# Kernel tuning notes

Hardware: AMD Instinct MI355X
Metric: run time of the kernel (lower is better)

## Reference

```python
import jax, jax.numpy as jnp
import numpy as np

B, D, K, DM = 4096, 64, 64, 512  # batch, latent_dim, num_charts, d_model
BALL_EPS = 1e-5


def _l2n(x):
    return x / (jnp.linalg.norm(x) + 1e-12)


def _spectral_scale(W, iters=5):
    # torch.nn.utils.spectral_norm semantics: power iteration with no-grad u,v,
    # gradient flows through W in sigma = u^T W v.
    Wd = jax.lax.stop_gradient(W)
    u = _l2n(jnp.ones((W.shape[0],), W.dtype))
    v = _l2n(Wd.T @ u)
    for _ in range(iters):
        v = _l2n(Wd.T @ u)
        u = _l2n(Wd @ v)
    sigma = u @ (W @ v)
    return W / sigma


def spectral_linear(x, W, b):
    return x @ _spectral_scale(W).T + b


def _project_to_ball(x):
    n = jnp.linalg.norm(x, axis=-1, keepdims=True)
    scale = jnp.minimum(1.0, (1.0 - BALL_EPS) / jnp.maximum(n, 1e-12))
    return x * scale


def _poincare_dist2(x, y):
    # x: [B, D] query positions, y: [B, K, D] chart centers -> squared geodesic dist [B, K]
    diff2 = jnp.sum((x[:, None, :] - y) ** 2, axis=-1)
    den = (1.0 - jnp.sum(x * x, axis=-1, keepdims=True)) * (1.0 - jnp.sum(y * y, axis=-1))
    arg = 1.0 + 2.0 * diff2 / jnp.maximum(den, 1e-12)
    d = jnp.arccosh(jnp.maximum(arg, 1.0 + 1e-7))
    return d * d


def covariant_attention(z_q, z_kv, x_q, x_k, x_v, Wq, bq, Wk, bk, Wv, bv, Wo, bo, geo_scale):
    # Single-head geodesic-biased attention (GeodesicConfig n_heads=1).
    q = x_q @ Wq.T + bq                               # [B, DM]
    k = jnp.einsum('bkd,ed->bke', x_k, Wk) + bk       # [B, K, DM]
    v = jnp.einsum('bkd,ed->bke', x_v, Wv) + bv       # [B, K, DM]
    scores = jnp.einsum('bd,bkd->bk', q, k) / jnp.sqrt(jnp.asarray(DM, q.dtype))
    scores = scores - geo_scale * _poincare_dist2(z_q, z_kv)
    attn = jax.nn.softmax(scores, axis=-1)            # [B, K]
    feat = jnp.einsum('bk,bkd->bd', attn, v)
    out = feat @ Wo.T + bo                            # [B, DM]
    return out, attn


def setup_inputs() -> dict:
    keys = jax.random.split(jax.random.key(0), 20)
    z = 0.05 * jax.random.normal(keys[0], (B, D), jnp.float32)      # inside unit ball
    rw = jax.nn.softmax(jax.random.normal(keys[1], (B, K), jnp.float32), axis=-1)
    chart_emb = 0.02 * jax.random.normal(keys[2], (K, DM), jnp.float32)
    cc = jax.random.normal(keys[3], (K, D), jnp.float32)
    chart_centers = 0.3 * (cc / jnp.linalg.norm(cc, axis=-1, keepdims=True))
    s = 0.02
    return {
        'z': z, 'rw': rw,
        'chart_emb': chart_emb, 'chart_centers': chart_centers,
        'zW': s * jax.random.normal(keys[4], (DM, D), jnp.float32),
        'zb': jnp.zeros((DM,), jnp.float32),
        'Wq': s * jax.random.normal(keys[5], (DM, DM), jnp.float32),
        'bq': jnp.zeros((DM,), jnp.float32),
        'Wk': s * jax.random.normal(keys[6], (DM, DM), jnp.float32),
        'bk': jnp.zeros((DM,), jnp.float32),
        'Wv': s * jax.random.normal(keys[7], (DM, DM), jnp.float32),
        'bv': jnp.zeros((DM,), jnp.float32),
        'Wo': s * jax.random.normal(keys[8], (DM, DM), jnp.float32),
        'bo': jnp.zeros((DM,), jnp.float32),
        'geo_scale': jnp.ones((), jnp.float32),
        'vW': s * jax.random.normal(keys[9], (1, DM), jnp.float32),
        'vb': jnp.zeros((1,), jnp.float32),
    }


def reference(z, rw, chart_emb, chart_centers, zW, zb, Wq, bq, Wk, bk, Wv, bv, Wo, bo, geo_scale, vW, vb):
    # ChartTokenizer: broadcast-multiply router weights with chart embeddings
    tokens_x = rw[:, :, None] * chart_emb[None]            # [B, K, DM]
    tokens_z = jnp.broadcast_to(_project_to_ball(chart_centers)[None], (z.shape[0], K, D))
    # z embedding (SpectralLinear)
    x_q = spectral_linear(z, zW, zb)                       # [B, DM]
    # critic covariant attention
    v_feat, _ = covariant_attention(z, tokens_z, x_q, tokens_x, tokens_x,
                                    Wq, bq, Wk, bk, Wv, bv, Wo, bo, geo_scale)
    # task value head (SpectralLinear -> scalar)
    return spectral_linear(v_feat, vW, vb)                 # [B, 1]
```

## Files before the change

### kernel.cpp

```cpp
#include <hip/hip_runtime.h>
#include <math.h>

#define WS_INV    0
#define WS_INVSV  1
#define WS_BOVW   2
#define WS_BVWO   3
#define WS_N2V    4
#define WS_COLSUM 64
#define WS_A      128
#define WS_WO0    4224
#define WS_QZB    4736
#define WS_CK0    5248
#define WS_CVW    5312
#define WS_NY2    5376
#define WS_YT     5440
#define WS_T1     16384
#define WS_V1     49152
#define WS_P1     81920
#define WS_GP     114688

#define PRE_LDSB  (36928 * 4)
#define MID_LDSB  (16384 * 4)

__device__ __forceinline__ float wave_sum(float x) {
#pragma unroll
    for (int o = 32; o; o >>= 1) x += __shfl_xor(x, o);
    return x;
}

__device__ __forceinline__ float block_sum512(float v, float* red) {
    float s = wave_sum(v);
    const int wid = threadIdx.x >> 6;
    __syncthreads();
    if ((threadIdx.x & 63) == 0) red[wid] = s;
    __syncthreads();
    float t2 = 0.0f;
#pragma unroll
    for (int i = 0; i < 8; ++i) t2 += red[i];
    return t2;
}

__global__ __launch_bounds__(512) void k_pre(
    const float* __restrict__ zW, const float* __restrict__ zb,
    const float* __restrict__ Wq, const float* __restrict__ bq,
    const float* __restrict__ Wk, const float* __restrict__ Wv,
    const float* __restrict__ Wo, const float* __restrict__ ce,
    const float* __restrict__ cc, const float* __restrict__ vW,
    const float* __restrict__ bo, float* __restrict__ ws)
{
    extern __shared__ float sm[];
    const int blk = blockIdx.x, t = threadIdx.x;
    const int lane = t & 63, w = t >> 6;

    if (blk < 128) {
        const int f0 = blk * 4;
        float* ces = sm;
        float* wkv = sm + 32832;
#pragma unroll 4
        for (int i = 0; i < 64; ++i) {
            const int idx = i * 512 + t;
            ces[(idx >> 9) * 513 + (idx & 511)] = ce[idx];
        }
        {
            const float4* Wk4 = (const float4*)Wk;
            const float4* Wv4 = (const float4*)Wv;
            float4* wkv4 = (float4*)wkv;
#pragma unroll
            for (int i = 0; i < 2; ++i) {
                const int idx = i * 512 + t;
                const int a = idx >> 7, c4 = idx & 127;
                wkv4[idx] = (a < 4) ? Wk4[(f0 + a) * 128 + c4]
                                    : Wv4[(f0 + a - 4) * 128 + c4];
            }
        }
        __syncthreads();
        float acc[8];
#pragma unroll
        for (int a = 0; a < 8; ++a) acc[a] = 0.0f;
        const int c0 = w * 64;
#pragma unroll 2
        for (int q4 = 0; q4 < 16; ++q4) {
            const int c = c0 + q4 * 4;
            const float cv0 = ces[lane * 513 + c + 0];
            const float cv1 = ces[lane * 513 + c + 1];
            const float cv2 = ces[lane * 513 + c + 2];
            const float cv3 = ces[lane * 513 + c + 3];
#pragma unroll
            for (int a = 0; a < 8; ++a) {
                const float4 wv4 = *(const float4*)&wkv[a * 512 + c];
                acc[a] = fmaf(wv4.x, cv0, acc[a]);
                acc[a] = fmaf(wv4.y, cv1, acc[a]);
                acc[a] = fmaf(wv4.z, cv2, acc[a]);
                acc[a] = fmaf(wv4.w, cv3, acc[a]);
            }
        }
        __syncthreads();
        float* part = sm;
#pragma unroll
        for (int a = 0; a < 8; ++a) part[(a * 8 + w) * 65 + lane] = acc[a];
        __syncthreads();
        {
            float s = 0.0f;
#pragma unroll
            for (int ww = 0; ww < 8; ++ww) s += part[(w * 8 + ww) * 65 + lane];
            if (w < 4) ws[WS_T1 + (f0 + w) * 64 + lane] = s;
            else       ws[WS_V1 + (f0 + w - 4) * 64 + lane] = s;
        }

    } else if (blk < 192) {
        const int f0 = (blk - 128) * 8;
        float* zl = sm;
        float* wq = sm + 32768;
        {
            const float4* zW4 = (const float4*)zW;
            float4* zl4 = (float4*)zl;
#pragma unroll 4
            for (int i = 0; i < 16; ++i) zl4[i * 512 + t] = zW4[i * 512 + t];
            const float4* Wq4 = (const float4*)Wq;
            float4* wq4 = (float4*)wq;
#pragma unroll
            for (int i = 0; i < 2; ++i)
                wq4[i * 512 + t] = Wq4[f0 * 128 + i * 512 + t];
        }
        __syncthreads();
        float acc[8];
#pragma unroll
        for (int a = 0; a < 8; ++a) acc[a] = 0.0f;
        const int e0 = w * 64;
#pragma unroll 2
        for (int q4 = 0; q4 < 16; ++q4) {
            const int e = e0 + q4 * 4;
            const float z0 = zl[(e + 0) * 64 + lane];
            const float z1 = zl[(e + 1) * 64 + lane];
            const float z2 = zl[(e + 2) * 64 + lane];
            const float z3 = zl[(e + 3) * 64 + lane];
#pragma unroll
            for (int fi = 0; fi < 8; ++fi) {
                const float4 q4v = *(const float4*)&wq[fi * 512 + e];
                acc[fi] = fmaf(q4v.x, z0, acc[fi]);
                acc[fi] = fmaf(q4v.y, z1, acc[fi]);
                acc[fi] = fmaf(q4v.z, z2, acc[fi]);
                acc[fi] = fmaf(q4v.w, z3, acc[fi]);
            }
        }
        __syncthreads();
        float* part = sm;
#pragma unroll
        for (int a = 0; a < 8; ++a) part[(a * 8 + w) * 65 + lane] = acc[a];
        __syncthreads();
        {
            float s = 0.0f;
#pragma unroll
            for (int ww = 0; ww < 8; ++ww) s += part[(w * 8 + ww) * 65 + lane];
            ws[WS_P1 + (f0 + w) * 64 + lane] = s;
        }

    } else if (blk < 200) {
        const int r0 = (blk - 192) * 8;
        float* zl = sm;
        {
            const float4* zW4 = (const float4*)zW;
            float4* zl4 = (float4*)zl;
#pragma unroll 4
            for (int i = 0; i < 16; ++i) zl4[i * 512 + t] = zW4[i * 512 + t];
        }
        __syncthreads();
        float acc[8];
#pragma unroll
        for (int a = 0; a < 8; ++a) acc[a] = 0.0f;
        float cs = 0.0f;
        const int e0 = w * 64;
#pragma unroll 2
        for (int q4 = 0; q4 < 16; ++q4) {
            const int e = e0 + q4 * 4;
#pragma unroll
            for (int j = 0; j < 4; ++j) {
                const float zv = zl[(e + j) * 64 + lane];
                cs += zv;
                const float4 b0 = *(const float4*)&zl[(e + j) * 64 + r0];
                const float4 b1 = *(const float4*)&zl[(e + j) * 64 + r0 + 4];
                acc[0] = fmaf(b0.x, zv, acc[0]);
                acc[1] = fmaf(b0.y, zv, acc[1]);
                acc[2] = fmaf(b0.z, zv, acc[2]);
                acc[3] = fmaf(b0.w, zv, acc[3]);
                acc[4] = fmaf(b1.x, zv, acc[4]);
                acc[5] = fmaf(b1.y, zv, acc[5]);
                acc[6] = fmaf(b1.z, zv, acc[6]);
                acc[7] = fmaf(b1.w, zv, acc[7]);
            }
        }
        __syncthreads();
        float* part = sm;
        float* part2 = sm + 4160;
#pragma unroll
        for (int a = 0; a < 8; ++a) part[(a * 8 + w) * 65 + lane] = acc[a];
        if (blk == 192) part2[w * 65 + lane] = cs;
        __syncthreads();
        {
            float s = 0.0f;
#pragma unroll
            for (int ww = 0; ww < 8; ++ww) s += part[(w * 8 + ww) * 65 + lane];
            ws[WS_A + (r0 + w) * 64 + lane] = s;
        }
        if (blk == 192 && t < 64) {
            float s = 0.0f;
#pragma unroll
            for (int ww = 0; ww < 8; ++ww) s += part2[ww * 65 + t];
            ws[WS_COLSUM + t] = s;
        }

    } else if (blk < 208) {
        const int f0 = (blk - 200) * 64;
        float zbr[8];
#pragma unroll
        for (int i = 0; i < 8; ++i) zbr[i] = zb[i * 64 + lane];
#pragma unroll
        for (int ff = 0; ff < 8; ++ff) {
            const int f = f0 + w * 8 + ff;
            float s = 0.0f;
#pragma unroll
            for (int i = 0; i < 8; ++i)
                s = fmaf(Wq[f * 512 + i * 64 + lane], zbr[i], s);
            s = wave_sum(s);
            if (lane == 0) ws[WS_QZB + f] = s + bq[f];
        }

    } else if (blk < 216) {
        const int e0 = (blk - 208) * 64;
        float s = 0.0f;
#pragma unroll 4
        for (int gi = 0; gi < 64; ++gi) {
            const int g = w * 64 + gi;
            s = fmaf(Wo[g * 512 + e0 + lane], vW[g], s);
        }
        float* part = sm;
        part[w * 65 + lane] = s;
        __syncthreads();
        if (t < 64) {
            float o = 0.0f;
#pragma unroll
            for (int ww = 0; ww < 8; ++ww) o += part[ww * 65 + t];
            ws[WS_WO0 + e0 + t] = o;
        }

    } else {
        float* red = sm;
        const float vwt = vW[t];
        const float n2v = block_sum512(vwt * vwt, red);
        if (t == 0) ws[WS_N2V] = n2v;
        const float bv_ = block_sum512(bo[t] * vwt, red);
        if (t == 0) ws[WS_BOVW] = bv_;
        if (t < 64) {
            float n2 = 0.0f;
            for (int dd = 0; dd < 64; ++dd) {
                const float c = cc[t * 64 + dd];
                n2 = fmaf(c, c, n2);
            }
            const float n = sqrtf(n2);
            const float scale = fminf(1.0f, (1.0f - 1e-5f) / fmaxf(n, 1e-12f));
            float s2 = 0.0f;
            for (int dd = 0; dd < 64; ++dd) {
                const float yv = cc[t * 64 + dd] * scale;
                ws[WS_YT + dd * 64 + t] = yv;
                s2 = fmaf(yv, yv, s2);
            }
            ws[WS_NY2 + t] = s2;
        }
    }
}

__global__ __launch_bounds__(512) void k_mid(
    const float* __restrict__ bv, float* __restrict__ ws)
{
    extern __shared__ float sm[];
    const int blk = blockIdx.x, t = threadIdx.x;
    const int lane = t & 63, w = t >> 6;

    if (blk == 0) {
        float* As = sm;
#pragma unroll
        for (int i = 0; i < 8; ++i) {
            const int idx = i * 512 + t;
            As[(idx >> 6) * 65 + (idx & 63)] = ws[WS_A + idx];
        }
        __syncthreads();
        if (w == 0) {
            const int d = lane;
            const float u0val = 1.0f / (sqrtf(512.0f) + 1e-12f);
            const float x = ws[WS_COLSUM + d] * u0val;
            const float nx = sqrtf(wave_sum(x * x));
            float v = x / (nx + 1e-12f);
            float mv;
            for (int it = 0; it < 4; ++it) {
                mv = 0.0f;
                for (int j = 0; j < 64; ++j)
                    mv = fmaf(As[j * 65 + d], __shfl(v, j), mv);
                const float s1 = wave_sum(mv * v);
                const float s2 = wave_sum(mv * mv);
                const float n = sqrtf(s1);
                const float inv1 = 1.0f / (n + 1e-12f);
                const float ny = sqrtf(s2) * inv1;
                v = mv * inv1 / (ny + 1e-12f);
            }
            mv = 0.0f;
            for (int j = 0; j < 64; ++j)
                mv = fmaf(As[j * 65 + d], __shfl(v, j), mv);
            const float n5sq = wave_sum(mv * v);
            const float n5 = sqrtf(n5sq);
            const float sig = n5sq / (n5 + 1e-12f);
            if (lane == 0) ws[WS_INV] = 1.0f / sig;
        } else if (w == 1) {
            float s = 0.0f;
#pragma unroll
            for (int i = 0; i < 8; ++i)
                s = fmaf(bv[i * 64 + lane], ws[WS_WO0 + i * 64 + lane], s);
            s = wave_sum(s);
            if (lane == 0) ws[WS_BVWO] = s;
        } else if (w == 2 && lane == 0) {
            const float n2 = ws[WS_N2V];
            const float rn = sqrtf(n2);
            float u = 1.0f / (1.0f + 1e-12f), s = 0.0f;
            for (int it = 0; it < 5; ++it) {
                const float nv = fabsf(u) * rn;
                const float vs = u / (nv + 1e-12f);
                s = n2 * vs;
                u = s / (fabsf(s) + 1e-12f);
            }
            ws[WS_INVSV] = 1.0f / (u * s);
        }

    } else if (blk < 3) {
        const int mat = (blk == 1) ? WS_V1 : WS_T1;
        const int vec = (blk == 1) ? WS_WO0 : WS_QZB;
        const int dst = (blk == 1) ? WS_CVW : WS_CK0;
        float s = 0.0f;
#pragma unroll 4
        for (int i = 0; i < 64; ++i) {
            const int e = w * 64 + i;
            s = fmaf(ws[mat + e * 64 + lane], ws[vec + e], s);
        }
        float* part = sm;
        part[w * 65 + lane] = s;
        __syncthreads();
        if (t < 64) {
            float o = 0.0f;
#pragma unroll
            for (int ww = 0; ww < 8; ++ww) o += part[ww * 65 + t];
            ws[dst + t] = o;
        }

    } else {
        const int p = blk - 3;
        const int f0 = p * 128;
        float* T1s = sm;
        float* P1s = sm + 8192;
        {
            const float4* a4 = (const float4*)&ws[WS_T1 + f0 * 64];
            const float4* b4 = (const float4*)&ws[WS_P1 + f0 * 64];
            float4* T14 = (float4*)T1s;
            float4* P14 = (float4*)P1s;
#pragma unroll
            for (int i = 0; i < 4; ++i) {
                T14[i * 512 + t] = a4[i * 512 + t];
                P14[i * 512 + t] = b4[i * 512 + t];
            }
        }
        __syncthreads();
        float acc[8];
#pragma unroll
        for (int j = 0; j < 8; ++j) acc[j] = 0.0f;
        const int d0 = w * 8;
#pragma unroll 2
        for (int f = 0; f < 128; ++f) {
            const float a = T1s[f * 64 + lane];
            const float4 p0 = *(const float4*)&P1s[f * 64 + d0];
            const float4 p1 = *(const float4*)&P1s[f * 64 + d0 + 4];
            acc[0] = fmaf(a, p0.x, acc[0]);
            acc[1] = fmaf(a, p0.y, acc[1]);
            acc[2] = fmaf(a, p0.z, acc[2]);
            acc[3] = fmaf(a, p0.w, acc[3]);
            acc[4] = fmaf(a, p1.x, acc[4]);
            acc[5] = fmaf(a, p1.y, acc[5]);
            acc[6] = fmaf(a, p1.z, acc[6]);
            acc[7] = fmaf(a, p1.w, acc[7]);
        }
#pragma unroll
        for (int j = 0; j < 8; ++j)
            ws[WS_GP + p * 4096 + (d0 + j) * 64 + lane] = acc[j];
    }
}

__global__ __launch_bounds__(256) void k_main(
    const float* __restrict__ z, const float* __restrict__ rw,
    const float* __restrict__ geo, const float* __restrict__ vb,
    const float* __restrict__ ws, float* __restrict__ out)
{
    __shared__ float sGt[4096];
    __shared__ float sYt[4096];
    __shared__ float sCvw[64], sCk0[64], sNy2[64], sSc[2];
    const int t = threadIdx.x;
    const float inv_s = ws[WS_INV];
    const float inv_sv = ws[WS_INVSV];
    for (int i = t; i < 4096; i += 256) {
        sGt[i] = inv_s * (ws[WS_GP + i] + ws[WS_GP + 4096 + i]
                        + ws[WS_GP + 8192 + i] + ws[WS_GP + 12288 + i]);
        sYt[i] = ws[WS_YT + i];
    }
    if (t < 64) {
        sCvw[t] = inv_sv * ws[WS_CVW + t];
        sCk0[t] = ws[WS_CK0 + t];
        sNy2[t] = ws[WS_NY2 + t];
    }
    if (t == 0) {
        sSc[0] = inv_sv * (ws[WS_BVWO] + ws[WS_BOVW]) + vb[0];
        sSc[1] = geo[0];
    }
    __syncthreads();
    const int wid = t >> 6, lane = t & 63;
    const float gs = sSc[1], cst = sSc[0];
    const float rs512 = 0.04419417382415922f;
#pragma unroll
    for (int r = 0; r < 4; ++r) {
        const int b = blockIdx.x * 16 + wid * 4 + r;
        const float zl = z[b * 64 + lane];
        const float rwk = rw[b * 64 + lane];
        float dot = 0.0f, diff2 = 0.0f, nz2 = 0.0f;
#pragma unroll 8
        for (int dd = 0; dd < 64; ++dd) {
            const float zd = __shfl(zl, dd);
            nz2 = fmaf(zd, zd, nz2);
            dot = fmaf(zd, sGt[dd * 64 + lane], dot);
            const float df = zd - sYt[dd * 64 + lane];
            diff2 = fmaf(df, df, diff2);
        }
        const float den = (1.0f - nz2) * (1.0f - sNy2[lane]);
        float arg = 1.0f + 2.0f * diff2 / fmaxf(den, 1e-12f);
        arg = fmaxf(arg, 1.0f + 1e-7f);
        const float dg = acoshf(arg);
        const float score = rwk * (dot + sCk0[lane]) * rs512 - gs * dg * dg;
        float m = score;
#pragma unroll
        for (int o = 32; o; o >>= 1) m = fmaxf(m, __shfl_xor(m, o));
        const float e = expf(score - m);
        float s1 = e, s2 = e * rwk * sCvw[lane];
#pragma unroll
        for (int o = 32; o; o >>= 1) { s1 += __shfl_xor(s1, o); s2 += __shfl_xor(s2, o); }
        if (lane == 0) out[b] = s2 / s1 + cst;
    }
}

extern "C" void kernel_launch(void* const* d_in, const int* in_sizes, int n_in,
                              void* d_out, int out_size, void* d_ws, size_t ws_size,
                              hipStream_t stream)
{
    (void)in_sizes; (void)n_in; (void)out_size; (void)ws_size;
    const float* z   = (const float*)d_in[0];
    const float* rw  = (const float*)d_in[1];
    const float* cem = (const float*)d_in[2];
    const float* cc  = (const float*)d_in[3];
    const float* zW  = (const float*)d_in[4];
    const float* zb  = (const float*)d_in[5];
    const float* Wq  = (const float*)d_in[6];
    const float* bq  = (const float*)d_in[7];
    const float* Wk  = (const float*)d_in[8];
    const float* Wv  = (const float*)d_in[10];
    const float* bv  = (const float*)d_in[11];
    const float* Wo  = (const float*)d_in[12];
    const float* bo  = (const float*)d_in[13];
    const float* geo = (const float*)d_in[14];
    const float* vW  = (const float*)d_in[15];
    const float* vb  = (const float*)d_in[16];
    float* ws  = (float*)d_ws;
    float* out = (float*)d_out;

    hipLaunchKernelGGL(k_pre,  dim3(217), dim3(512), PRE_LDSB, stream,
                       zW, zb, Wq, bq, Wk, Wv, Wo, cem, cc, vW, bo, ws);
    hipLaunchKernelGGL(k_mid,  dim3(7),   dim3(512), MID_LDSB, stream, bv, ws);
    hipLaunchKernelGGL(k_main, dim3(256), dim3(256), 0, stream,
                       z, rw, geo, vb, ws, out);
}
```

Before: 32.90 us.

## Fuse three kernels into one cooperative kernel with grid-wide syncs

Folds the three sequential kernels (precompute, mid reductions, main attention) into one cooperative launch of 256 blocks of 512 threads, with grid syncs between phases. The goal is to remove two kernel-launch gaps and their inter-kernel idle time. Phase C is retuned to 512 threads per block with 2 rows per wave. A fallback to the three-kernel path remains if cooperative launch is unsupported or fails. The trade-off is the cost of grid syncs, ~144KB of dynamic LDS per block limiting residency, and host attribute queries on every call.

```diff
diff --git a/kernel.cpp b/kernel.cpp
--- a/kernel.cpp
+++ b/kernel.cpp
@@ -1,5 +1,8 @@
 #include <hip/hip_runtime.h>
+#include <hip/hip_cooperative_groups.h>
 #include <math.h>
+
+namespace cg = cooperative_groups;
 
 #define WS_INV    0
 #define WS_INVSV  1
@@ -19,8 +22,8 @@
 #define WS_P1     81920
 #define WS_GP     114688
 
-#define PRE_LDSB  (36928 * 4)
-#define MID_LDSB  (16384 * 4)
+#define FUSED_LDSB (36928 * 4)
+#define MAIN_LDSB  (8448 * 4)
 
 __device__ __forceinline__ float wave_sum(float x) {
 #pragma unroll
@@ -40,7 +43,8 @@
     return t2;
 }
 
-__global__ __launch_bounds__(512) void k_pre(
+__device__ __forceinline__ void phaseA(
+    const int blk, const int t, float* sm,
     const float* __restrict__ zW, const float* __restrict__ zb,
     const float* __restrict__ Wq, const float* __restrict__ bq,
     const float* __restrict__ Wk, const float* __restrict__ Wv,
@@ -48,8 +52,6 @@
     const float* __restrict__ cc, const float* __restrict__ vW,
     const float* __restrict__ bo, float* __restrict__ ws)
 {
-    extern __shared__ float sm[];
-    const int blk = blockIdx.x, t = threadIdx.x;
     const int lane = t & 63, w = t >> 6;
 
     if (blk < 128) {
@@ -243,7 +245,7 @@
             ws[WS_WO0 + e0 + t] = o;
         }
 
-    } else {
+    } else if (blk == 216) {
         float* red = sm;
         const float vwt = vW[t];
         const float n2v = block_sum512(vwt * vwt, red);
@@ -269,11 +271,10 @@
     }
 }
 
-__global__ __launch_bounds__(512) void k_mid(
+__device__ __forceinline__ void phaseB(
+    const int blk, const int t, float* sm,
     const float* __restrict__ bv, float* __restrict__ ws)
 {
-    extern __shared__ float sm[];
-    const int blk = blockIdx.x, t = threadIdx.x;
     const int lane = t & 63, w = t >> 6;
 
     if (blk == 0) {
@@ -349,7 +350,7 @@
             ws[dst + t] = o;
         }
 
-    } else {
+    } else if (blk < 7) {
         const int p = blk - 3;
         const int f0 = p * 128;
         float* T1s = sm;
@@ -390,18 +391,21 @@
     }
 }
 
-__global__ __launch_bounds__(256) void k_main(
+__device__ __forceinline__ void phaseC(
+    const int blk, const int t, float* sm,
     const float* __restrict__ z, const float* __restrict__ rw,
     const float* __restrict__ geo, const float* __restrict__ vb,
     const float* __restrict__ ws, float* __restrict__ out)
 {
-    __shared__ float sGt[4096];
-    __shared__ float sYt[4096];
-    __shared__ float sCvw[64], sCk0[64], sNy2[64], sSc[2];
-    const int t = threadIdx.x;
+    float* sGt  = sm;
+    float* sYt  = sm + 4096;
+    float* sCvw = sm + 8192;
+    float* sCk0 = sm + 8256;
+    float* sNy2 = sm + 8320;
+    float* sSc  = sm + 8384;
     const float inv_s = ws[WS_INV];
     const float inv_sv = ws[WS_INVSV];
-    for (int i = t; i < 4096; i += 256) {
+    for (int i = t; i < 4096; i += 512) {
         sGt[i] = inv_s * (ws[WS_GP + i] + ws[WS_GP + 4096 + i]
                         + ws[WS_GP + 8192 + i] + ws[WS_GP + 12288 + i]);
         sYt[i] = ws[WS_YT + i];
@@ -420,8 +424,8 @@
     const float gs = sSc[1], cst = sSc[0];
     const float rs512 = 0.04419417382415922f;
 #pragma unroll
-    for (int r = 0; r < 4; ++r) {
-        const int b = blockIdx.x * 16 + wid * 4 + r;
+    for (int r = 0; r < 2; ++r) {
+        const int b = blk * 16 + wid * 2 + r;
         const float zl = z[b * 64 + lane];
         const float rwk = rw[b * 64 + lane];
         float dot = 0.0f, diff2 = 0.0f, nz2 = 0.0f;
@@ -447,6 +451,45 @@
         for (int o = 32; o; o >>= 1) { s1 += __shfl_xor(s1, o); s2 += __shfl_xor(s2, o); }
         if (lane == 0) out[b] = s2 / s1 + cst;
     }
+}
+
+__global__ __launch_bounds__(512, 2) void k_fused(
+    const float* zW, const float* zb, const float* Wq, const float* bq,
+    const float* Wk, const float* Wv, const float* Wo, const float* ce,
+    const float* cc, const float* vW, const float* bo, const float* bv,
+    const float* z, const float* rw, const float* geo, const float* vb,
+    float* ws, float* out)
+{
+    extern __shared__ float sm[];
+    const int blk = blockIdx.x, t = threadIdx.x;
+    phaseA(blk, t, sm, zW, zb, Wq, bq, Wk, Wv, Wo, ce, cc, vW, bo, ws);
+    cg::this_grid().sync();
+    phaseB(blk, t, sm, bv, ws);
+    cg::this_grid().sync();
+    phaseC(blk, t, sm, z, rw, geo, vb, ws, out);
+}
+
+__global__ __launch_bounds__(512) void k_pre(
+    const float* zW, const float* zb, const float* Wq, const float* bq,
+    const float* Wk, const float* Wv, const float* Wo, const float* ce,
+    const float* cc, const float* vW, const float* bo, float* ws)
+{
+    extern __shared__ float sm[];
+    phaseA(blockIdx.x, threadIdx.x, sm, zW, zb, Wq, bq, Wk, Wv, Wo, ce, cc, vW, bo, ws);
+}
+
+__global__ __launch_bounds__(512) void k_mid(const float* bv, float* ws)
+{
+    extern __shared__ float sm[];
+    phaseB(blockIdx.x, threadIdx.x, sm, bv, ws);
+}
+
+__global__ __launch_bounds__(512) void k_main(
+    const float* z, const float* rw, const float* geo, const float* vb,
+    const float* ws, float* out)
+{
+    extern __shared__ float sm[];
+    phaseC(blockIdx.x, threadIdx.x, sm, z, rw, geo, vb, ws, out);
 }
 
 extern "C" void kernel_launch(void* const* d_in, const int* in_sizes, int n_in,
@@ -473,9 +516,24 @@
     float* ws  = (float*)d_ws;
     float* out = (float*)d_out;
 
-    hipLaunchKernelGGL(k_pre,  dim3(217), dim3(512), PRE_LDSB, stream,
+    int coop = 0, dev = 0;
+    hipGetDevice(&dev);
+    hipDeviceGetAttribute(&coop, hipDeviceAttributeCooperativeLaunch, dev);
+    if (coop) {
+        void* args[] = {
+            (void*)&zW, (void*)&zb, (void*)&Wq, (void*)&bq,
+            (void*)&Wk, (void*)&Wv, (void*)&Wo, (void*)&cem,
+            (void*)&cc, (void*)&vW, (void*)&bo, (void*)&bv,
+            (void*)&z,  (void*)&rw, (void*)&geo, (void*)&vb,
+            (void*)&ws, (void*)&out };
+        hipError_t e = hipLaunchCooperativeKernel((const void*)k_fused,
+                                                  dim3(256), dim3(512),
+                                                  args, FUSED_LDSB, stream);
+        if (e == hipSuccess) return;
+    }
+    hipLaunchKernelGGL(k_pre,  dim3(217), dim3(512), FUSED_LDSB, stream,
                        zW, zb, Wq, bq, Wk, Wv, Wo, cem, cc, vW, bo, ws);
-    hipLaunchKernelGGL(k_mid,  dim3(7),   dim3(512), MID_LDSB, stream, bv, ws);
-    hipLaunchKernelGGL(k_main, dim3(256), dim3(256), 0, stream,
+    hipLaunchKernelGGL(k_mid,  dim3(7),   dim3(512), FUSED_LDSB, stream, bv, ws);
+    hipLaunchKernelGGL(k_main, dim3(256), dim3(512), MAIN_LDSB, stream,
                        z, rw, geo, vb, ws, out);
 }
```

Measured after the change: 97.44 us. 2.96x slower.

## Fold mid kernel into main kernel, recomputing power iteration and projections per block

Applied to the files above, without the earlier changes.

Removes the separate k_mid launch by having every k_main block redundantly compute the spectral-norm power iteration, bias dot products and the T1/P1 projections. The G matrix is no longer materialized; instead each block computes z·P1 and then contracts with T1 for its 16 rows. The k_pre chart-embedding load is also vectorized to float4. This trades one kernel launch and a serialization point for substantial redundant per-block work (reading T1, V1 and P1 from global memory in all 256 blocks) and a larger LDS footprint.

```diff
diff --git a/kernel.cpp b/kernel.cpp
--- a/kernel.cpp
+++ b/kernel.cpp
@@ -1,26 +1,33 @@
 #include <hip/hip_runtime.h>
 #include <math.h>
 
-#define WS_INV    0
-#define WS_INVSV  1
 #define WS_BOVW   2
-#define WS_BVWO   3
 #define WS_N2V    4
 #define WS_COLSUM 64
 #define WS_A      128
 #define WS_WO0    4224
 #define WS_QZB    4736
-#define WS_CK0    5248
-#define WS_CVW    5312
 #define WS_NY2    5376
 #define WS_YT     5440
 #define WS_T1     16384
 #define WS_V1     49152
 #define WS_P1     81920
-#define WS_GP     114688
 
 #define PRE_LDSB  (36928 * 4)
-#define MID_LDSB  (16384 * 4)
+
+#define YL    0
+#define ZL    8192
+#define AL    9216
+#define QZBL  13376
+#define WO0L  13888
+#define YTL   14400
+#define NY2L  18496
+#define PD    18560
+#define PCV   26176
+#define PBV   26624
+#define MISC  26631
+#define K2F   26640
+#define K2_LDSB (K2F * 4)
 
 __device__ __forceinline__ float wave_sum(float x) {
 #pragma unroll
@@ -56,10 +63,16 @@
         const int f0 = blk * 4;
         float* ces = sm;
         float* wkv = sm + 32832;
+        {
+            const float4* ce4 = (const float4*)ce;
 #pragma unroll 4
-        for (int i = 0; i < 64; ++i) {
-            const int idx = i * 512 + t;
-            ces[(idx >> 9) * 513 + (idx & 511)] = ce[idx];
+            for (int i = 0; i < 16; ++i) {
+                const int idx4 = i * 512 + t;
+                const int k = idx4 >> 7, c4 = idx4 & 127;
+                const float4 v = ce4[idx4];
+                float* dst = &ces[k * 513 + c4 * 4];
+                dst[0] = v.x; dst[1] = v.y; dst[2] = v.z; dst[3] = v.w;
+            }
         }
         {
             const float4* Wk4 = (const float4*)Wk;
@@ -269,54 +282,77 @@
     }
 }
 
-__global__ __launch_bounds__(512) void k_mid(
-    const float* __restrict__ bv, float* __restrict__ ws)
+__global__ __launch_bounds__(512) void k_main(
+    const float* __restrict__ z, const float* __restrict__ rw,
+    const float* __restrict__ geo, const float* __restrict__ vb,
+    const float* __restrict__ bv, const float* __restrict__ ws,
+    float* __restrict__ out)
 {
     extern __shared__ float sm[];
-    const int blk = blockIdx.x, t = threadIdx.x;
+    const int t = threadIdx.x;
     const int lane = t & 63, w = t >> 6;
-
-    if (blk == 0) {
-        float* As = sm;
-#pragma unroll
-        for (int i = 0; i < 8; ++i) {
-            const int idx = i * 512 + t;
-            As[(idx >> 6) * 65 + (idx & 63)] = ws[WS_A + idx];
-        }
-        __syncthreads();
-        if (w == 0) {
-            const int d = lane;
-            const float u0val = 1.0f / (sqrtf(512.0f) + 1e-12f);
-            const float x = ws[WS_COLSUM + d] * u0val;
-            const float nx = sqrtf(wave_sum(x * x));
-            float v = x / (nx + 1e-12f);
-            float mv;
-            for (int it = 0; it < 4; ++it) {
-                mv = 0.0f;
-                for (int j = 0; j < 64; ++j)
-                    mv = fmaf(As[j * 65 + d], __shfl(v, j), mv);
-                const float s1 = wave_sum(mv * v);
-                const float s2 = wave_sum(mv * mv);
-                const float n = sqrtf(s1);
-                const float inv1 = 1.0f / (n + 1e-12f);
-                const float ny = sqrtf(s2) * inv1;
-                v = mv * inv1 / (ny + 1e-12f);
-            }
-            mv = 0.0f;
+    const int b0 = blockIdx.x * 16;
+
+#pragma unroll
+    for (int i = 0; i < 2; ++i) sm[ZL + i * 512 + t] = z[b0 * 64 + i * 512 + t];
+#pragma unroll
+    for (int i = 0; i < 8; ++i) {
+        const int idx = i * 512 + t;
+        sm[AL + (idx >> 6) * 65 + (idx & 63)] = ws[WS_A + idx];
+        sm[YTL + idx] = ws[WS_YT + idx];
+    }
+    sm[QZBL + t] = ws[WS_QZB + t];
+    sm[WO0L + t] = ws[WS_WO0 + t];
+    if (t < 64) sm[NY2L + t] = ws[WS_NY2 + t];
+    if (t == 0) {
+        sm[MISC + 2] = ws[WS_BOVW];
+        sm[MISC + 3] = vb[0];
+        sm[MISC + 4] = geo[0];
+    }
+    __syncthreads();
+
+    {
+        float acc[16];
+#pragma unroll
+        for (int r = 0; r < 16; ++r) acc[r] = 0.0f;
+        const float* p1 = ws + WS_P1 + t * 64;
+#pragma unroll 4
+        for (int dq = 0; dq < 16; ++dq) {
+            const float4 pv = *(const float4*)(p1 + dq * 4);
+#pragma unroll
+            for (int r = 0; r < 16; ++r) {
+                const float4 zv = *(const float4*)&sm[ZL + r * 64 + dq * 4];
+                acc[r] = fmaf(pv.x, zv.x, acc[r]);
+                acc[r] = fmaf(pv.y, zv.y, acc[r]);
+                acc[r] = fmaf(pv.z, zv.z, acc[r]);
+                acc[r] = fmaf(pv.w, zv.w, acc[r]);
+            }
+        }
+#pragma unroll
+        for (int r = 0; r < 16; ++r) sm[YL + r * 512 + t] = acc[r];
+    }
+    __syncthreads();
+
+    if (w == 0) {
+        float wv = ws[WS_COLSUM + lane];
+#pragma unroll
+        for (int it = 0; it < 4; ++it) {
+            float mv = 0.0f;
             for (int j = 0; j < 64; ++j)
-                mv = fmaf(As[j * 65 + d], __shfl(v, j), mv);
-            const float n5sq = wave_sum(mv * v);
-            const float n5 = sqrtf(n5sq);
-            const float sig = n5sq / (n5 + 1e-12f);
-            if (lane == 0) ws[WS_INV] = 1.0f / sig;
-        } else if (w == 1) {
-            float s = 0.0f;
-#pragma unroll
-            for (int i = 0; i < 8; ++i)
-                s = fmaf(bv[i * 64 + lane], ws[WS_WO0 + i * 64 + lane], s);
-            s = wave_sum(s);
-            if (lane == 0) ws[WS_BVWO] = s;
-        } else if (w == 2 && lane == 0) {
+                mv = fmaf(sm[AL + j * 65 + lane], __shfl(wv, j), mv);
+            wv = mv;
+        }
+        const float s8 = wave_sum(wv * wv);
+        float mv = 0.0f;
+        for (int j = 0; j < 64; ++j)
+            mv = fmaf(sm[AL + j * 65 + lane], __shfl(wv, j), mv);
+        const float s9 = wave_sum(mv * wv);
+        const float den = sqrtf(s8) + 1e-12f;
+        const float n5sq = s9 / (den * den);
+        const float n5 = sqrtf(n5sq);
+        const float sig = n5sq / (n5 + 1e-12f);
+        if (lane == 0) sm[MISC + 0] = 1.0f / sig;
+        if (lane == 0) {
             const float n2 = ws[WS_N2V];
             const float rn = sqrtf(n2);
             float u = 1.0f / (1.0f + 1e-12f), s = 0.0f;
@@ -326,123 +362,93 @@
                 s = n2 * vs;
                 u = s / (fabsf(s) + 1e-12f);
             }
-            ws[WS_INVSV] = 1.0f / (u * s);
-        }
-
-    } else if (blk < 3) {
-        const int mat = (blk == 1) ? WS_V1 : WS_T1;
-        const int vec = (blk == 1) ? WS_WO0 : WS_QZB;
-        const int dst = (blk == 1) ? WS_CVW : WS_CK0;
-        float s = 0.0f;
-#pragma unroll 4
-        for (int i = 0; i < 64; ++i) {
-            const int e = w * 64 + i;
-            s = fmaf(ws[mat + e * 64 + lane], ws[vec + e], s);
-        }
-        float* part = sm;
-        part[w * 65 + lane] = s;
-        __syncthreads();
-        if (t < 64) {
-            float o = 0.0f;
-#pragma unroll
-            for (int ww = 0; ww < 8; ++ww) o += part[ww * 65 + t];
-            ws[dst + t] = o;
-        }
-
+            sm[MISC + 1] = 1.0f / (u * s);
+        }
     } else {
-        const int p = blk - 3;
-        const int f0 = p * 128;
-        float* T1s = sm;
-        float* P1s = sm + 8192;
-        {
-            const float4* a4 = (const float4*)&ws[WS_T1 + f0 * 64];
-            const float4* b4 = (const float4*)&ws[WS_P1 + f0 * 64];
-            float4* T14 = (float4*)T1s;
-            float4* P14 = (float4*)P1s;
-#pragma unroll
-            for (int i = 0; i < 4; ++i) {
-                T14[i * 512 + t] = a4[i * 512 + t];
-                P14[i * 512 + t] = b4[i * 512 + t];
-            }
-        }
-        __syncthreads();
-        float acc[8];
-#pragma unroll
-        for (int j = 0; j < 8; ++j) acc[j] = 0.0f;
-        const int d0 = w * 8;
-#pragma unroll 2
-        for (int f = 0; f < 128; ++f) {
-            const float a = T1s[f * 64 + lane];
-            const float4 p0 = *(const float4*)&P1s[f * 64 + d0];
-            const float4 p1 = *(const float4*)&P1s[f * 64 + d0 + 4];
-            acc[0] = fmaf(a, p0.x, acc[0]);
-            acc[1] = fmaf(a, p0.y, acc[1]);
-            acc[2] = fmaf(a, p0.z, acc[2]);
-            acc[3] = fmaf(a, p0.w, acc[3]);
-            acc[4] = fmaf(a, p1.x, acc[4]);
-            acc[5] = fmaf(a, p1.y, acc[5]);
-            acc[6] = fmaf(a, p1.z, acc[6]);
-            acc[7] = fmaf(a, p1.w, acc[7]);
-        }
-#pragma unroll
-        for (int j = 0; j < 8; ++j)
-            ws[WS_GP + p * 4096 + (d0 + j) * 64 + lane] = acc[j];
-    }
-}
-
-__global__ __launch_bounds__(256) void k_main(
-    const float* __restrict__ z, const float* __restrict__ rw,
-    const float* __restrict__ geo, const float* __restrict__ vb,
-    const float* __restrict__ ws, float* __restrict__ out)
-{
-    __shared__ float sGt[4096];
-    __shared__ float sYt[4096];
-    __shared__ float sCvw[64], sCk0[64], sNy2[64], sSc[2];
-    const int t = threadIdx.x;
-    const float inv_s = ws[WS_INV];
-    const float inv_sv = ws[WS_INVSV];
-    for (int i = t; i < 4096; i += 256) {
-        sGt[i] = inv_s * (ws[WS_GP + i] + ws[WS_GP + 4096 + i]
-                        + ws[WS_GP + 8192 + i] + ws[WS_GP + 12288 + i]);
-        sYt[i] = ws[WS_YT + i];
-    }
-    if (t < 64) {
-        sCvw[t] = inv_sv * ws[WS_CVW + t];
-        sCk0[t] = ws[WS_CK0 + t];
-        sNy2[t] = ws[WS_NY2 + t];
-    }
-    if (t == 0) {
-        sSc[0] = inv_sv * (ws[WS_BVWO] + ws[WS_BOVW]) + vb[0];
-        sSc[1] = geo[0];
+        const int m = w - 1;
+        const int fs = m * 76;
+        const int fe = (m == 6) ? 512 : fs + 76;
+        float dotr[16];
+#pragma unroll
+        for (int r = 0; r < 16; ++r) dotr[r] = 0.0f;
+        float ck0p = 0.0f;
+        for (int f = fs; f < fe; f += 4) {
+            const float t0 = ws[WS_T1 + (f + 0) * 64 + lane];
+            const float t1 = ws[WS_T1 + (f + 1) * 64 + lane];
+            const float t2 = ws[WS_T1 + (f + 2) * 64 + lane];
+            const float t3 = ws[WS_T1 + (f + 3) * 64 + lane];
+            const float4 qv = *(const float4*)&sm[QZBL + f];
+            ck0p = fmaf(t0, qv.x, ck0p);
+            ck0p = fmaf(t1, qv.y, ck0p);
+            ck0p = fmaf(t2, qv.z, ck0p);
+            ck0p = fmaf(t3, qv.w, ck0p);
+#pragma unroll
+            for (int r = 0; r < 16; ++r) {
+                const float4 yv = *(const float4*)&sm[YL + r * 512 + f];
+                dotr[r] = fmaf(t0, yv.x, dotr[r]);
+                dotr[r] = fmaf(t1, yv.y, dotr[r]);
+                dotr[r] = fmaf(t2, yv.z, dotr[r]);
+                dotr[r] = fmaf(t3, yv.w, dotr[r]);
+            }
+        }
+        float cvwp = 0.0f;
+        for (int e = fs; e < fe; ++e)
+            cvwp = fmaf(ws[WS_V1 + e * 64 + lane], sm[WO0L + e], cvwp);
+        float bvw = 0.0f;
+        for (int e = fs; e < fe; ++e)
+            bvw = fmaf(bv[e], sm[WO0L + e], bvw);
+#pragma unroll
+        for (int r = 0; r < 16; ++r)
+            sm[PD + m * 1088 + r * 64 + lane] = dotr[r];
+        sm[PD + m * 1088 + 1024 + lane] = ck0p;
+        sm[PCV + m * 64 + lane] = cvwp;
+        if (lane == 0) sm[PBV + m] = bvw;
     }
     __syncthreads();
-    const int wid = t >> 6, lane = t & 63;
-    const float gs = sSc[1], cst = sSc[0];
+
+    const float inv_s = sm[MISC + 0];
+    const float inv_sv = sm[MISC + 1];
+    float bvwo = 0.0f;
+#pragma unroll
+    for (int m = 0; m < 7; ++m) bvwo += sm[PBV + m];
+    const float cst = inv_sv * (bvwo + sm[MISC + 2]) + sm[MISC + 3];
+    const float gs = sm[MISC + 4];
+    float ck0 = 0.0f, cvw = 0.0f;
+#pragma unroll
+    for (int m = 0; m < 7; ++m) {
+        ck0 += sm[PD + m * 1088 + 1024 + lane];
+        cvw += sm[PCV + m * 64 + lane];
+    }
+    cvw *= inv_sv;
+    const float ny2 = sm[NY2L + lane];
     const float rs512 = 0.04419417382415922f;
 #pragma unroll
-    for (int r = 0; r < 4; ++r) {
-        const int b = blockIdx.x * 16 + wid * 4 + r;
-        const float zl = z[b * 64 + lane];
+    for (int rr = 0; rr < 2; ++rr) {
+        const int r = w * 2 + rr;
+        const int b = b0 + r;
         const float rwk = rw[b * 64 + lane];
-        float dot = 0.0f, diff2 = 0.0f, nz2 = 0.0f;
+        float dacc = 0.0f;
+#pragma unroll
+        for (int m = 0; m < 7; ++m) dacc += sm[PD + m * 1088 + r * 64 + lane];
+        const float dot = inv_s * dacc;
+        float diff2 = 0.0f, nz2 = 0.0f;
 #pragma unroll 8
         for (int dd = 0; dd < 64; ++dd) {
-            const float zd = __shfl(zl, dd);
+            const float zd = sm[ZL + r * 64 + dd];
             nz2 = fmaf(zd, zd, nz2);
-            dot = fmaf(zd, sGt[dd * 64 + lane], dot);
-            const float df = zd - sYt[dd * 64 + lane];
+            const float df = zd - sm[YTL + dd * 64 + lane];
             diff2 = fmaf(df, df, diff2);
         }
-        const float den = (1.0f - nz2) * (1.0f - sNy2[lane]);
+        const float den = (1.0f - nz2) * (1.0f - ny2);
         float arg = 1.0f + 2.0f * diff2 / fmaxf(den, 1e-12f);
         arg = fmaxf(arg, 1.0f + 1e-7f);
         const float dg = acoshf(arg);
-        const float score = rwk * (dot + sCk0[lane]) * rs512 - gs * dg * dg;
-        float m = score;
-#pragma unroll
-        for (int o = 32; o; o >>= 1) m = fmaxf(m, __shfl_xor(m, o));
-        const float e = expf(score - m);
-        float s1 = e, s2 = e * rwk * sCvw[lane];
+        const float score = rwk * (dot + ck0) * rs512 - gs * dg * dg;
+        float mx = score;
+#pragma unroll
+        for (int o = 32; o; o >>= 1) mx = fmaxf(mx, __shfl_xor(mx, o));
+        const float e = expf(score - mx);
+        float s1 = e, s2 = e * rwk * cvw;
 #pragma unroll
         for (int o = 32; o; o >>= 1) { s1 += __shfl_xor(s1, o); s2 += __shfl_xor(s2, o); }
         if (lane == 0) out[b] = s2 / s1 + cst;
@@ -475,7 +481,6 @@
 
     hipLaunchKernelGGL(k_pre,  dim3(217), dim3(512), PRE_LDSB, stream,
                        zW, zb, Wq, bq, Wk, Wv, Wo, cem, cc, vW, bo, ws);
-    hipLaunchKernelGGL(k_mid,  dim3(7),   dim3(512), MID_LDSB, stream, bv, ws);
-    hipLaunchKernelGGL(k_main, dim3(256), dim3(256), 0, stream,
-                       z, rw, geo, vb, ws, out);
+    hipLaunchKernelGGL(k_main, dim3(256), dim3(512), K2_LDSB, stream,
+                       z, rw, geo, vb, bv, ws, out);
 }
```

Measured after the change: 66.23 us. +101.3%, slower.

## Fuse mid-stage into main kernel with atomic flag spin-wait

Applied to the files above, without the earlier changes.

Merges the 7-block k_mid stage into k_main: the first 7 blocks do the former mid work and then bump an agent-scope atomic counter. All 256 blocks preload the per-call constants, spin on that counter, then run the per-row attention with 512 threads per block. This removes one kernel launch boundary and lets the constant loads overlap the mid work, but it relies on the 7 producer blocks being scheduled while the others spin. The chart-embedding load in k_pre is also switched to float4 reads.

```diff
diff --git a/kernel.cpp b/kernel.cpp
--- a/kernel.cpp
+++ b/kernel.cpp
@@ -6,6 +6,7 @@
 #define WS_BOVW   2
 #define WS_BVWO   3
 #define WS_N2V    4
+#define WS_FLAG   8
 #define WS_COLSUM 64
 #define WS_A      128
 #define WS_WO0    4224
@@ -20,7 +21,7 @@
 #define WS_GP     114688
 
 #define PRE_LDSB  (36928 * 4)
-#define MID_LDSB  (16384 * 4)
+#define K2_LDSB   (16384 * 4)
 
 __device__ __forceinline__ float wave_sum(float x) {
 #pragma unroll
@@ -56,10 +57,16 @@
         const int f0 = blk * 4;
         float* ces = sm;
         float* wkv = sm + 32832;
+        {
+            const float4* ce4 = (const float4*)ce;
 #pragma unroll 4
-        for (int i = 0; i < 64; ++i) {
-            const int idx = i * 512 + t;
-            ces[(idx >> 9) * 513 + (idx & 511)] = ce[idx];
+            for (int i = 0; i < 16; ++i) {
+                const int idx4 = i * 512 + t;
+                const int k = idx4 >> 7, c4 = idx4 & 127;
+                const float4 v = ce4[idx4];
+                float* dst = &ces[k * 513 + c4 * 4];
+                dst[0] = v.x; dst[1] = v.y; dst[2] = v.z; dst[3] = v.w;
+            }
         }
         {
             const float4* Wk4 = (const float4*)Wk;
@@ -249,7 +256,10 @@
         const float n2v = block_sum512(vwt * vwt, red);
         if (t == 0) ws[WS_N2V] = n2v;
         const float bv_ = block_sum512(bo[t] * vwt, red);
-        if (t == 0) ws[WS_BOVW] = bv_;
+        if (t == 0) {
+            ws[WS_BOVW] = bv_;
+            ((int*)ws)[WS_FLAG] = 0;
+        }
         if (t < 64) {
             float n2 = 0.0f;
             for (int dd = 0; dd < 64; ++dd) {
@@ -269,159 +279,179 @@
     }
 }
 
-__global__ __launch_bounds__(512) void k_mid(
-    const float* __restrict__ bv, float* __restrict__ ws)
+__global__ __launch_bounds__(512) void k_main(
+    const float* __restrict__ z, const float* __restrict__ rw,
+    const float* __restrict__ geo, const float* __restrict__ vb,
+    const float* __restrict__ bv, float* __restrict__ ws,
+    float* __restrict__ out)
 {
     extern __shared__ float sm[];
     const int blk = blockIdx.x, t = threadIdx.x;
     const int lane = t & 63, w = t >> 6;
-
-    if (blk == 0) {
-        float* As = sm;
-#pragma unroll
-        for (int i = 0; i < 8; ++i) {
-            const int idx = i * 512 + t;
-            As[(idx >> 6) * 65 + (idx & 63)] = ws[WS_A + idx];
-        }
-        __syncthreads();
-        if (w == 0) {
-            const int d = lane;
-            const float u0val = 1.0f / (sqrtf(512.0f) + 1e-12f);
-            const float x = ws[WS_COLSUM + d] * u0val;
-            const float nx = sqrtf(wave_sum(x * x));
-            float v = x / (nx + 1e-12f);
-            float mv;
-            for (int it = 0; it < 4; ++it) {
+    int* flag = (int*)ws + WS_FLAG;
+
+    if (blk < 7) {
+        if (blk == 0) {
+            float* As = sm;
+#pragma unroll
+            for (int i = 0; i < 8; ++i) {
+                const int idx = i * 512 + t;
+                As[(idx >> 6) * 65 + (idx & 63)] = ws[WS_A + idx];
+            }
+            __syncthreads();
+            if (w == 0) {
+                const int d = lane;
+                const float u0val = 1.0f / (sqrtf(512.0f) + 1e-12f);
+                const float x = ws[WS_COLSUM + d] * u0val;
+                const float nx = sqrtf(wave_sum(x * x));
+                float v = x / (nx + 1e-12f);
+                float mv;
+                for (int it = 0; it < 4; ++it) {
+                    mv = 0.0f;
+                    for (int j = 0; j < 64; ++j)
+                        mv = fmaf(As[j * 65 + d], __shfl(v, j), mv);
+                    const float s1 = wave_sum(mv * v);
+                    const float s2 = wave_sum(mv * mv);
+                    const float n = sqrtf(s1);
+                    const float inv1 = 1.0f / (n + 1e-12f);
+                    const float ny = sqrtf(s2) * inv1;
+                    v = mv * inv1 / (ny + 1e-12f);
+                }
                 mv = 0.0f;
                 for (int j = 0; j < 64; ++j)
                     mv = fmaf(As[j * 65 + d], __shfl(v, j), mv);
-                const float s1 = wave_sum(mv * v);
-                const float s2 = wave_sum(mv * mv);
-                const float n = sqrtf(s1);
-                const float inv1 = 1.0f / (n + 1e-12f);
-                const float ny = sqrtf(s2) * inv1;
-                v = mv * inv1 / (ny + 1e-12f);
-            }
-            mv = 0.0f;
-            for (int j = 0; j < 64; ++j)
-                mv = fmaf(As[j * 65 + d], __shfl(v, j), mv);
-            const float n5sq = wave_sum(mv * v);
-            const float n5 = sqrtf(n5sq);
-            const float sig = n5sq / (n5 + 1e-12f);
-            if (lane == 0) ws[WS_INV] = 1.0f / sig;
-        } else if (w == 1) {
+                const float n5sq = wave_sum(mv * v);
+                const float n5 = sqrtf(n5sq);
+                const float sig = n5sq / (n5 + 1e-12f);
+                if (lane == 0) ws[WS_INV] = 1.0f / sig;
+            } else if (w == 1) {
+                float s = 0.0f;
+#pragma unroll
+                for (int i = 0; i < 8; ++i)
+                    s = fmaf(bv[i * 64 + lane], ws[WS_WO0 + i * 64 + lane], s);
+                s = wave_sum(s);
+                if (lane == 0) ws[WS_BVWO] = s;
+            } else if (w == 2 && lane == 0) {
+                const float n2 = ws[WS_N2V];
+                const float rn = sqrtf(n2);
+                float u = 1.0f / (1.0f + 1e-12f), s = 0.0f;
+                for (int it = 0; it < 5; ++it) {
+                    const float nv = fabsf(u) * rn;
+                    const float vs = u / (nv + 1e-12f);
+                    s = n2 * vs;
+                    u = s / (fabsf(s) + 1e-12f);
+                }
+                ws[WS_INVSV] = 1.0f / (u * s);
+            }
+
+        } else if (blk < 3) {
+            const int mat = (blk == 1) ? WS_V1 : WS_T1;
+            const int vec = (blk == 1) ? WS_WO0 : WS_QZB;
+            const int dst = (blk == 1) ? WS_CVW : WS_CK0;
             float s = 0.0f;
-#pragma unroll
-            for (int i = 0; i < 8; ++i)
-                s = fmaf(bv[i * 64 + lane], ws[WS_WO0 + i * 64 + lane], s);
-            s = wave_sum(s);
-            if (lane == 0) ws[WS_BVWO] = s;
-        } else if (w == 2 && lane == 0) {
-            const float n2 = ws[WS_N2V];
-            const float rn = sqrtf(n2);
-            float u = 1.0f / (1.0f + 1e-12f), s = 0.0f;
-            for (int it = 0; it < 5; ++it) {
-                const float nv = fabsf(u) * rn;
-                const float vs = u / (nv + 1e-12f);
-                s = n2 * vs;
-                u = s / (fabsf(s) + 1e-12f);
-            }
-            ws[WS_INVSV] = 1.0f / (u * s);
-        }
-
-    } else if (blk < 3) {
-        const int mat = (blk == 1) ? WS_V1 : WS_T1;
-        const int vec = (blk == 1) ? WS_WO0 : WS_QZB;
-        const int dst = (blk == 1) ? WS_CVW : WS_CK0;
-        float s = 0.0f;
 #pragma unroll 4
-        for (int i = 0; i < 64; ++i) {
-            const int e = w * 64 + i;
-            s = fmaf(ws[mat + e * 64 + lane], ws[vec + e], s);
-        }
-        float* part = sm;
-        part[w * 65 + lane] = s;
-        __syncthreads();
-        if (t < 64) {
-            float o = 0.0f;
-#pragma unroll
-            for (int ww = 0; ww < 8; ++ww) o += part[ww * 65 + t];
-            ws[dst + t] = o;
-        }
-
-    } else {
-        const int p = blk - 3;
-        const int f0 = p * 128;
-        float* T1s = sm;
-        float* P1s = sm + 8192;
-        {
-            const float4* a4 = (const float4*)&ws[WS_T1 + f0 * 64];
-            const float4* b4 = (const float4*)&ws[WS_P1 + f0 * 64];
-            float4* T14 = (float4*)T1s;
-            float4* P14 = (float4*)P1s;
-#pragma unroll
-            for (int i = 0; i < 4; ++i) {
-                T14[i * 512 + t] = a4[i * 512 + t];
-                P14[i * 512 + t] = b4[i * 512 + t];
-            }
-        }
-        __syncthreads();
-        float acc[8];
-#pragma unroll
-        for (int j = 0; j < 8; ++j) acc[j] = 0.0f;
-        const int d0 = w * 8;
+            for (int i = 0; i < 64; ++i) {
+                const int e = w * 64 + i;
+                s = fmaf(ws[mat + e * 64 + lane], ws[vec + e], s);
+            }
+            float* part = sm;
+            part[w * 65 + lane] = s;
+            __syncthreads();
+            if (t < 64) {
+                float o = 0.0f;
+#pragma unroll
+                for (int ww = 0; ww < 8; ++ww) o += part[ww * 65 + t];
+                ws[dst + t] = o;
+            }
+
+        } else {
+            const int p = blk - 3;
+            const int f0 = p * 128;
+            float* T1s = sm;
+            float* P1s = sm + 8192;
+            {
+                const float4* a4 = (const float4*)&ws[WS_T1 + f0 * 64];
+                const float4* b4 = (const float4*)&ws[WS_P1 + f0 * 64];
+                float4* T14 = (float4*)T1s;
+                float4* P14 = (float4*)P1s;
+#pragma unroll
+                for (int i = 0; i < 4; ++i) {
+                    T14[i * 512 + t] = a4[i * 512 + t];
+                    P14[i * 512 + t] = b4[i * 512 + t];
+                }
+            }
+            __syncthreads();
+            float acc[8];
+#pragma unroll
+            for (int j = 0; j < 8; ++j) acc[j] = 0.0f;
+            const int d0 = w * 8;
 #pragma unroll 2
-        for (int f = 0; f < 128; ++f) {
-            const float a = T1s[f * 64 + lane];
-            const float4 p0 = *(const float4*)&P1s[f * 64 + d0];
-            const float4 p1 = *(const float4*)&P1s[f * 64 + d0 + 4];
-            acc[0] = fmaf(a, p0.x, acc[0]);
-            acc[1] = fmaf(a, p0.y, acc[1]);
-            acc[2] = fmaf(a, p0.z, acc[2]);
-            acc[3] = fmaf(a, p0.w, acc[3]);
-            acc[4] = fmaf(a, p1.x, acc[4]);
-            acc[5] = fmaf(a, p1.y, acc[5]);
-            acc[6] = fmaf(a, p1.z, acc[6]);
-            acc[7] = fmaf(a, p1.w, acc[7]);
-        }
-#pragma unroll
-        for (int j = 0; j < 8; ++j)
-            ws[WS_GP + p * 4096 + (d0 + j) * 64 + lane] = acc[j];
+            for (int f = 0; f < 128; ++f) {
+                const float a = T1s[f * 64 + lane];
+                const float4 p0 = *(const float4*)&P1s[f * 64 + d0];
+                const float4 p1 = *(const float4*)&P1s[f * 64 + d0 + 4];
+                acc[0] = fmaf(a, p0.x, acc[0]);
+                acc[1] = fmaf(a, p0.y, acc[1]);
+                acc[2] = fmaf(a, p0.z, acc[2]);
+                acc[3] = fmaf(a, p0.w, acc[3]);
+                acc[4] = fmaf(a, p1.x, acc[4]);
+                acc[5] = fmaf(a, p1.y, acc[5]);
+                acc[6] = fmaf(a, p1.z, acc[6]);
+                acc[7] = fmaf(a, p1.w, acc[7]);
+            }
+#pragma unroll
+            for (int j = 0; j < 8; ++j)
+                ws[WS_GP + p * 4096 + (d0 + j) * 64 + lane] = acc[j];
+        }
+        __syncthreads();
+        if (t == 0) {
+            __threadfence();
+            __hip_atomic_fetch_add(flag, 1, __ATOMIC_RELEASE,
+                                   __HIP_MEMORY_SCOPE_AGENT);
+        }
+        __syncthreads();
     }
-}
-
-__global__ __launch_bounds__(256) void k_main(
-    const float* __restrict__ z, const float* __restrict__ rw,
-    const float* __restrict__ geo, const float* __restrict__ vb,
-    const float* __restrict__ ws, float* __restrict__ out)
-{
-    __shared__ float sGt[4096];
-    __shared__ float sYt[4096];
-    __shared__ float sCvw[64], sCk0[64], sNy2[64], sSc[2];
-    const int t = threadIdx.x;
+
+    float* sGt  = sm;
+    float* sYt  = sm + 4096;
+    float* sCvw = sm + 8192;
+    float* sCk0 = sm + 8256;
+    float* sNy2 = sm + 8320;
+    float* sSc  = sm + 8384;
+    for (int i = t; i < 4096; i += 512) sYt[i] = ws[WS_YT + i];
+    if (t < 64) sNy2[t] = ws[WS_NY2 + t];
+    if (t == 1) sSc[1] = geo[0];
+    __syncthreads();
+
+    if (t == 0) {
+        while (__hip_atomic_load(flag, __ATOMIC_ACQUIRE,
+                                 __HIP_MEMORY_SCOPE_AGENT) < 7) {
+            __builtin_amdgcn_s_sleep(16);
+        }
+    }
+    __syncthreads();
+    __threadfence();
+
     const float inv_s = ws[WS_INV];
     const float inv_sv = ws[WS_INVSV];
-    for (int i = t; i < 4096; i += 256) {
+    for (int i = t; i < 4096; i += 512) {
         sGt[i] = inv_s * (ws[WS_GP + i] + ws[WS_GP + 4096 + i]
                         + ws[WS_GP + 8192 + i] + ws[WS_GP + 12288 + i]);
-        sYt[i] = ws[WS_YT + i];
     }
     if (t < 64) {
         sCvw[t] = inv_sv * ws[WS_CVW + t];
         sCk0[t] = ws[WS_CK0 + t];
-        sNy2[t] = ws[WS_NY2 + t];
     }
-    if (t == 0) {
+    if (t == 0)
         sSc[0] = inv_sv * (ws[WS_BVWO] + ws[WS_BOVW]) + vb[0];
-        sSc[1] = geo[0];
-    }
     __syncthreads();
-    const int wid = t >> 6, lane = t & 63;
+
     const float gs = sSc[1], cst = sSc[0];
     const float rs512 = 0.04419417382415922f;
 #pragma unroll
-    for (int r = 0; r < 4; ++r) {
-        const int b = blockIdx.x * 16 + wid * 4 + r;
+    for (int rr = 0; rr < 2; ++rr) {
+        const int r = w * 2 + rr;
+        const int b = blk * 16 + r;
         const float zl = z[b * 64 + lane];
         const float rwk = rw[b * 64 + lane];
         float dot = 0.0f, diff2 = 0.0f, nz2 = 0.0f;
@@ -438,10 +468,10 @@
         arg = fmaxf(arg, 1.0f + 1e-7f);
         const float dg = acoshf(arg);
         const float score = rwk * (dot + sCk0[lane]) * rs512 - gs * dg * dg;
-        float m = score;
-#pragma unroll
-        for (int o = 32; o; o >>= 1) m = fmaxf(m, __shfl_xor(m, o));
-        const float e = expf(score - m);
+        float mx = score;
+#pragma unroll
+        for (int o = 32; o; o >>= 1) mx = fmaxf(mx, __shfl_xor(mx, o));
+        const float e = expf(score - mx);
         float s1 = e, s2 = e * rwk * sCvw[lane];
 #pragma unroll
         for (int o = 32; o; o >>= 1) { s1 += __shfl_xor(s1, o); s2 += __shfl_xor(s2, o); }
@@ -475,7 +505,6 @@
 
     hipLaunchKernelGGL(k_pre,  dim3(217), dim3(512), PRE_LDSB, stream,
                        zW, zb, Wq, bq, Wk, Wv, Wo, cem, cc, vW, bo, ws);
-    hipLaunchKernelGGL(k_mid,  dim3(7),   dim3(512), MID_LDSB, stream, bv, ws);
-    hipLaunchKernelGGL(k_main, dim3(256), dim3(256), 0, stream,
-                       z, rw, geo, vb, ws, out);
+    hipLaunchKernelGGL(k_main, dim3(256), dim3(512), K2_LDSB, stream,
+                       z, rw, geo, vb, bv, ws, out);
 }
```

Result: slower. 81.24 us (+146.9%).
